# Performance work log

Hardware: AMD Instinct MI355X
Metric: run time of the kernel (lower is better)

Reference implementation:

```python
import jax, jax.numpy as jnp
import numpy as np
from jax import lax

D_MODEL = 200
N_LAYER = 12
NHEADS = 8
HEADDIM = 50
D_STATE = 64
D_INNER = 2 * D_MODEL            # 400
CONV_DIM = D_INNER + 2 * D_STATE  # 528 (ngroups=1)
D_IN_PROJ = 2 * D_INNER + 2 * D_STATE + NHEADS  # 936
D_CONV = 4
EPS = 1e-5


def rmsnorm(x, w):
    v = jnp.mean(jnp.square(x), axis=-1, keepdims=True)
    return x * lax.rsqrt(v + EPS) * w


def groupnorm(x, groups, g, b):
    B, C, H, W = x.shape
    xg = x.reshape(B, groups, C // groups, H, W)
    mu = jnp.mean(xg, axis=(2, 3, 4), keepdims=True)
    var = jnp.mean(jnp.square(xg - mu), axis=(2, 3, 4), keepdims=True)
    xn = ((xg - mu) * lax.rsqrt(var + EPS)).reshape(B, C, H, W)
    return xn * g[:, None, None] + b[:, None, None]


def patch_embed(x, pe_conv_w, proj_in_w, gn_g, gn_b, spec_w):
    b, c, l, d = x.shape
    # time path: 'b c l d' -> (b, 1, c*l, d), conv -> (b, 25, c*l, 8)
    time_x = x.reshape(b, 1, c * l, d)
    t = lax.conv_general_dilated(time_x, proj_in_w, (1, 25), ((0, 0), (24, 24)),
                                 dimension_numbers=('NCHW', 'OIHW', 'NCHW'))
    t = jax.nn.gelu(groupnorm(t, 5, gn_g, gn_b), approximate=False)
    time_emb = t.transpose(0, 2, 1, 3).reshape(b, c, l, D_MODEL)
    # freq path: rfft over patch dim, norm='forward'
    spec = jnp.abs(jnp.fft.rfft(x, axis=-1, norm='forward'))  # (b,c,l,101)
    spec_emb = jnp.einsum('bclf,df->bcld', spec, spec_w)
    patch = time_emb + spec_emb
    # depthwise 7x7 positional conv over (d, c, l)
    pos = lax.conv_general_dilated(patch.transpose(0, 3, 1, 2), pe_conv_w, (1, 1),
                                   ((3, 3), (3, 3)),
                                   dimension_numbers=('NCHW', 'OIHW', 'NCHW'),
                                   feature_group_count=D_MODEL)
    return patch + pos.transpose(0, 2, 3, 1)


def ssd_scan(xh, dt, B, C, A, D):
    # xh: (b,l,h,p)  dt: (b,l,h)  B,C: (b,l,n)  A,D: (h,)
    b, l, h, p = xh.shape

    def step(state, inp):
        x_t, dt_t, B_t, C_t = inp
        dA = jnp.exp(dt_t * A)  # (b,h)
        state = state * dA[:, :, None, None] + \
            (dt_t[:, :, None, None] * x_t[:, :, :, None]) * B_t[:, None, None, :]
        y = jnp.einsum('bhpn,bn->bhp', state, C_t)
        return state, y

    state0 = jnp.zeros((b, h, p, D_STATE), xh.dtype)
    _, ys = lax.scan(step, state0,
                     (xh.transpose(1, 0, 2, 3), dt.transpose(1, 0, 2),
                      B.transpose(1, 0, 2), C.transpose(1, 0, 2)))
    return ys.transpose(1, 0, 2, 3) + xh * D[None, None, :, None]


def mamba2(u, in_w, conv_w, conv_b, dt_bias, A_log, D, gn_w, out_w):
    b, l, _ = u.shape
    zxbcdt = u @ in_w.T  # (b,l,936)
    z = zxbcdt[..., :D_INNER]
    xBC = zxbcdt[..., D_INNER:D_INNER + CONV_DIM]
    dt = jax.nn.softplus(zxbcdt[..., D_INNER + CONV_DIM:] + dt_bias)  # (b,l,8)
    # causal depthwise conv1d, kernel 4
    xc = lax.conv_general_dilated(xBC.transpose(0, 2, 1), conv_w, (1,), ((D_CONV - 1, 0),),
                                  dimension_numbers=('NCH', 'OIH', 'NCH'),
                                  feature_group_count=CONV_DIM)
    xBC = jax.nn.silu((xc + conv_b[:, None]).transpose(0, 2, 1))
    x = xBC[..., :D_INNER].reshape(b, l, NHEADS, HEADDIM)
    Bm = xBC[..., D_INNER:D_INNER + D_STATE]
    Cm = xBC[..., D_INNER + D_STATE:]
    y = ssd_scan(x, dt, Bm, Cm, -jnp.exp(A_log), D).reshape(b, l, D_INNER)
    y = rmsnorm(y * jax.nn.silu(z), gn_w)  # RMSNormGated, norm_before_gate=False
    return y @ out_w.T


@jax.checkpoint
def layer(hidden, residual, norm_w, in_w, conv_w, conv_b, dt_bias, A_log, D, gn_w, out_w):
    residual = hidden + residual
    hidden = mamba2(rmsnorm(residual, norm_w), in_w, conv_w, conv_b, dt_bias, A_log, D, gn_w, out_w)
    return hidden, residual


def forward(x, pe_conv_w, proj_in_w, gn_g, gn_b, spec_w, norm_w, in_proj_w, conv_w, conv_b,
            dt_bias, A_log, D, gnorm_w, out_proj_w, norm_f_w, head_w, head_b):
    b, c, l, d = x.shape
    hidden = patch_embed(x, pe_conv_w, proj_in_w, gn_g, gn_b, spec_w).reshape(b, c * l, d)
    residual = jnp.zeros_like(hidden)
    for i in range(N_LAYER):
        hidden, residual = layer(hidden, residual, norm_w[i], in_proj_w[i], conv_w[i],
                                 conv_b[i], dt_bias[i], A_log[i], D[i], gnorm_w[i], out_proj_w[i])
    hidden = rmsnorm(hidden + residual, norm_f_w).reshape(b, c, l, d)
    return hidden @ head_w.T + head_b


def setup_inputs():
    key = jax.random.key(0)
    ks = jax.random.split(key, 12)
    B, CH, L, P = 16, 19, 30, 200

    def g(k, shape, scale):
        return jax.random.normal(k, shape, jnp.float32) * scale

    dt = jax.random.uniform(ks[8], (N_LAYER, NHEADS), jnp.float32, 1e-3, 0.1)
    return {
        'x': g(ks[0], (B, CH, L, P), 1.0),
        'pe_conv_w': g(ks[1], (D_MODEL, 1, 7, 7), 0.15),
        'proj_in_w': g(ks[2], (25, 1, 1, 49), 0.14),
        'gn_g': jnp.ones(25, jnp.float32),
        'gn_b': jnp.zeros(25, jnp.float32),
        'spec_w': g(ks[3], (D_MODEL, 101), 0.1),
        'norm_w': jnp.ones((N_LAYER, D_MODEL), jnp.float32),
        'in_proj_w': g(ks[4], (N_LAYER, D_IN_PROJ, D_MODEL), 0.07),
        'conv_w': g(ks[5], (N_LAYER, CONV_DIM, 1, D_CONV), 0.4),
        'conv_b': jnp.zeros((N_LAYER, CONV_DIM), jnp.float32),
        'dt_bias': jnp.log(jnp.expm1(dt)),
        'A_log': jnp.log(jax.random.uniform(ks[9], (N_LAYER, NHEADS), jnp.float32, 1.0, 16.0)),
        'D': jnp.ones((N_LAYER, NHEADS), jnp.float32),
        'gnorm_w': jnp.ones((N_LAYER, D_INNER), jnp.float32),
        'out_proj_w': g(ks[6], (N_LAYER, D_MODEL, D_INNER), 0.05),
        'norm_f_w': jnp.ones(D_MODEL, jnp.float32),
        'head_w': g(ks[7], (D_MODEL, D_MODEL), 0.07),
        'head_b': jnp.zeros(D_MODEL, jnp.float32),
    }


def reference(x, pe_conv_w, proj_in_w, gn_g, gn_b, spec_w, norm_w, in_proj_w, conv_w, conv_b,
              dt_bias, A_log, D, gnorm_w, out_proj_w, norm_f_w, head_w, head_b):
    return forward(x, pe_conv_w, proj_in_w, gn_g, gn_b, spec_w, norm_w, in_proj_w, conv_w,
                   conv_b, dt_bias, A_log, D, gnorm_w, out_proj_w, norm_f_w, head_w, head_b)
```

## Files before the change

### kernel.cpp

```cpp
#include <hip/hip_runtime.h>
#include <hip/hip_bf16.h>
#include <math.h>

#define D_MODEL   200
#define N_LAYER   12
#define NHEADS    8
#define HEADDIM   50
#define D_STATE   64
#define D_INNER   400
#define CONV_DIM  528
#define D_IN_PROJ 936
#define D_CONV    4
#define EPS       1e-5f

#define BATCH 16
#define CH    19
#define LLEN  30
#define SEQ   570
#define NTOK  9120
#define NFREQ 101

typedef __attribute__((ext_vector_type(8))) short s8v;
typedef __attribute__((ext_vector_type(4))) float f32x4;

// ... 166 lines not shown
}

__global__ __launch_bounds__(256) void time_conv_kernel(
    const float* __restrict__ x, const float* __restrict__ pw,
    float* __restrict__ traw)
{
    int br = blockIdx.x;
    __shared__ float xr[200];
    if (threadIdx.x < 200) xr[threadIdx.x] = x[(size_t)br * 200 + threadIdx.x];
    __syncthreads();
    if (threadIdx.x < 200) {
        int oc = threadIdx.x >> 3, j = threadIdx.x & 7;
        int start = j * 25 - 24;
        float acc = 0.f;
#pragma unroll
        for (int k = 0; k < 49; k++) {
            int d = start + k;
            if (d >= 0 && d < 200) acc = fmaf(xr[d], pw[oc * 49 + k], acc);
        }
        int b = br / SEQ, row = br % SEQ;
        traw[(((size_t)b * 25 + oc) * SEQ + row) * 8 + j] = acc;
    }
}

__global__ __launch_bounds__(256) void gn_stats_kernel(
    const float* __restrict__ traw, float* __restrict__ stats)
{
    int bg = blockIdx.x;
    int b = bg / 5, g = bg % 5;
    const float* base = traw + ((size_t)b * 25 + g * 5) * SEQ * 8;
    float s = 0.f, q = 0.f;
    for (int i = threadIdx.x; i < 5 * SEQ * 8; i += 256) {
        float v = base[i];
        s += v; q = fmaf(v, v, q);
    }
    __shared__ float rs[4], rq[4];
    int lane = threadIdx.x & 63, w = threadIdx.x >> 6;
#pragma unroll
    for (int o = 32; o; o >>= 1) { s += __shfl_xor(s, o, 64); q += __shfl_xor(q, o, 64); }
    if (lane == 0) { rs[w] = s; rq[w] = q; }
    __syncthreads();
    if (threadIdx.x == 0) {
        float S = rs[0] + rs[1] + rs[2] + rs[3];
        float Q = rq[0] + rq[1] + rq[2] + rq[3];
        float inv = 1.f / (5.f * SEQ * 8.f);
        float mean = S * inv;
        float var = Q * inv - mean * mean;
        stats[bg * 2] = mean;
        stats[bg * 2 + 1] = rsqrtf(var + EPS);
    }
}

__global__ __launch_bounds__(256) void gn_gelu_kernel(
    const float* __restrict__ traw, const float* __restrict__ stats,
    const float* __restrict__ gn_g, const float* __restrict__ gn_b,
    float* __restrict__ patch)
{
    int idx = blockIdx.x * 256 + threadIdx.x;
    if (idx >= NTOK * 200) return;
    int d = idx % 200;
    int row = (idx / 200) % SEQ;
    int b = idx / (200 * SEQ);
    int oc = d >> 3, j = d & 7;
    float v = traw[(((size_t)b * 25 + oc) * SEQ + row) * 8 + j];
    int g = oc / 5;
    float mean = stats[(b * 5 + g) * 2];
    float rstd = stats[(b * 5 + g) * 2 + 1];
    v = (v - mean) * rstd * gn_g[oc] + gn_b[oc];
    float ge = 0.5f * v * (1.f + erff(v * 0.70710678118654752f));
    patch[idx] = ge;
}

__global__ __launch_bounds__(256) void dft_init_kernel(float* __restrict__ CS)
{
    int idx = blockIdx.x * 256 + threadIdx.x;
    if (idx >= 202 * 200) return;
    int f = idx / 200, d = idx % 200;
    int fr = (f < NFREQ) ? f : (f - NFREQ);
    int m = (fr * d) % 200;
    float ang = -6.283185307179586f * (float)m * (1.f / 200.f);
    CS[idx] = (f < NFREQ) ? cosf(ang) : sinf(ang);
}

__global__ __launch_bounds__(256) void dft_init_bf_kernel(short* __restrict__ CS)
{
    int idx = blockIdx.x * 256 + threadIdx.x;
    if (idx >= 202 * 224) return;
    int f = idx / 224, d = idx - f * 224;
    short out = 0;
    if (d < 200) {
        int fr = (f < NFREQ) ? f : (f - NFREQ);
        int m = (fr * d) % 200;
        float ang = -6.283185307179586f * (float)m * (1.f / 200.f);
        out = f2bf((f < NFREQ) ? cosf(ang) : sinf(ang));
    }
    CS[idx] = out;
}

__global__ __launch_bounds__(256) void mag_kernel(
    const float* __restrict__ cs_out, float* __restrict__ magv)
{
    int idx = blockIdx.x * 256 + threadIdx.x;
    if (idx >= NTOK * NFREQ) return;
    int m = idx / NFREQ, f = idx % NFREQ;
    float re = cs_out[(size_t)m * 202 + f];
    float im = cs_out[(size_t)m * 202 + NFREQ + f];
    magv[idx] = sqrtf(re * re + im * im) * 0.005f;
}

__global__ __launch_bounds__(256) void mag_bf_kernel(
    const float* __restrict__ cs_out, short* __restrict__ magv)
{
    int idx = blockIdx.x * 256 + threadIdx.x;
    if (idx >= NTOK * 128) return;
    int m = idx >> 7, f = idx & 127;
    short out = 0;
    if (f < NFREQ) {
        float re = cs_out[(size_t)m * 202 + f];
        float im = cs_out[(size_t)m * 202 + NFREQ + f];
        out = f2bf(sqrtf(re * re + im * im) * 0.005f);
    }
    magv[idx] = out;
}

__global__ __launch_bounds__(256) void pe_conv3_kernel(
    const float* __restrict__ patch, const float* __restrict__ pw,
    float* __restrict__ hidden)
{
    int b = blockIdx.x, dc = blockIdx.y, ct = blockIdx.z;
    int d0 = dc * 16, c0 = ct * 4;
    __shared__ float pl[10 * 30 * 16];
    __shared__ float wl[49 * 16];
    int tid = threadIdx.x;
    int dd = tid & 15;
    int d = d0 + dd;

    for (int i = tid; i < 10 * 30 * 16; i += 256) {
        int ddl = i & 15, r = i >> 4;
        int l = r % 30, cr = r / 30;
        int cc = c0 + cr - 3, dl = d0 + ddl;
        pl[i] = (cc >= 0 && cc < CH && dl < 200)
                    ? patch[((size_t)(b * CH + cc) * LLEN + l) * 200 + dl] : 0.f;
    }
    for (int i = tid; i < 49 * 16; i += 256) {
        int k = i >> 4, dl = d0 + (i & 15);
        wl[i] = (dl < 200) ? pw[(size_t)dl * 49 + k] : 0.f;
    }
    __syncthreads();

    float wreg[49];
#pragma unroll
    for (int k = 0; k < 49; k++) wreg[k] = wl[k * 16 + dd];

    for (int o = tid; o < 4 * 30 * 16; o += 256) {
        int r2 = o >> 4;
        int l = r2 % 30, ci = r2 / 30;
        int c = c0 + ci;
        if (c >= CH) continue;
        float acc = pl[((ci + 3) * 30 + l) * 16 + dd];
#pragma unroll
        for (int i = 0; i < 7; i++) {
#pragma unroll
            for (int j = 0; j < 7; j++) {
                int ll = l + j - 3;
                if (ll < 0 || ll >= LLEN) continue;
                acc = fmaf(pl[((ci + i) * 30 + ll) * 16 + dd], wreg[i * 7 + j], acc);
            }
        }
        if (d < 200) hidden[((size_t)(b * CH + c) * LLEN + l) * 200 + d] = acc;
    }
}

__global__ __launch_bounds__(64) void add_rmsnorm_kernel(
    const float* __restrict__ hidden, float* __restrict__ residual,
    const float* __restrict__ wn, float* __restrict__ u,
    short* __restrict__ ubf, int first)
{
    int m = blockIdx.x;
    int lane = threadIdx.x;
    const float* hr = hidden + (size_t)m * 200;
    float* rr = residual + (size_t)m * 200;
    float v[4];
    float ss = 0.f;
#pragma unroll
    for (int i = 0; i < 4; i++) {
        int k = lane + i * 64;
        float xv = 0.f;
        if (k < 200) {
            xv = hr[k] + (first ? 0.f : rr[k]);
            rr[k] = xv;
        }
        v[i] = xv;
        ss = fmaf(xv, xv, ss);
    }
#pragma unroll
    for (int o = 32; o; o >>= 1) ss += __shfl_xor(ss, o, 64);
    float rstd = rsqrtf(ss * (1.f / 200.f) + EPS);
#pragma unroll
    for (int i = 0; i < 4; i++) {
        int k = lane + i * 64;
        float val = v[i] * rstd * ((k < 200) ? wn[k] : 0.f);
        if (k < 200 && u) u[(size_t)m * 200 + k] = val;
        if (ubf) {
            if (k < 200) ubf[(size_t)m * 224 + k] = f2bf(val);
            else if (k < 224) ubf[(size_t)m * 224 + k] = 0;
        }
    }
}

__global__ __launch_bounds__(256) void norm_dt_kernel(
    const float* __restrict__ hidden, float* __restrict__ residual,
    const float* __restrict__ wn, short* __restrict__ ubf,
    const float* __restrict__ Win, const float* __restrict__ dt_bias,
    float* __restrict__ dtb, int layer, int first)
{
    int m = blockIdx.x;
    int tid = threadIdx.x;
    __shared__ float su[200];
    __shared__ float rs[4];
    float xv = 0.f;
    if (tid < 200) {
        xv = hidden[(size_t)m * 200 + tid] + (first ? 0.f : residual[(size_t)m * 200 + tid]);
        residual[(size_t)m * 200 + tid] = xv;
    }
    float ss = xv * xv;
#pragma unroll
    for (int o = 32; o; o >>= 1) ss += __shfl_xor(ss, o, 64);
    int lane = tid & 63, w = tid >> 6;
    if (lane == 0) rs[w] = ss;
    __syncthreads();
    float rstd = rsqrtf((rs[0] + rs[1] + rs[2] + rs[3]) * (1.f / 200.f) + EPS);
    if (tid < 200) {
        float val = xv * rstd * wn[tid];
        su[tid] = val;
        ubf[(size_t)m * 224 + tid] = f2bf(val);
    } else if (tid < 224) {
        ubf[(size_t)m * 224 + tid] = 0;
    }
    __syncthreads();
    int h = tid >> 5, l = tid & 31;
    const float* wr = Win + (size_t)layer * D_IN_PROJ * 200 + (size_t)(928 + h) * 200;
    float s = 0.f;
    for (int k = l; k < 200; k += 32) s = fmaf(su[k], wr[k], s);
    s += __shfl_xor(s, 16, 32);
    s += __shfl_xor(s, 8, 32);
    s += __shfl_xor(s, 4, 32);
    s += __shfl_xor(s, 2, 32);
    s += __shfl_xor(s, 1, 32);
    if (l == 0) {
        float raw = s + dt_bias[layer * NHEADS + h];
        dtb[(size_t)m * NHEADS + h] = (raw > 20.f) ? raw : log1pf(expf(raw));
    }
}

__global__ __launch_bounds__(256) void dt_gemv_kernel(
    const float* __restrict__ u, const float* __restrict__ Win,
    const float* __restrict__ dt_bias, float* __restrict__ dtb, int layer)
{
    int tid = threadIdx.x;
    int tok = blockIdx.x * 4 + (tid >> 6);
    int head = (tid >> 3) & 7;
    int l8 = tid & 7;
    const float* ur = u + (size_t)tok * 200;
    const float* wr = Win + (size_t)layer * D_IN_PROJ * 200 + (size_t)(928 + head) * 200;
    float s = 0.f;
    for (int k = l8; k < 200; k += 8) s = fmaf(ur[k], wr[k], s);
    s += __shfl_xor(s, 1, 64);
    s += __shfl_xor(s, 2, 64);
    s += __shfl_xor(s, 4, 64);
    if (l8 == 0) {
        float raw = s + dt_bias[layer * NHEADS + head];
        dtb[(size_t)tok * NHEADS + head] = (raw > 20.f) ? raw : log1pf(expf(raw));
    }
}

__global__ __launch_bounds__(256) void dtconv2_kernel(
    const float* __restrict__ zxbcdt, const float* __restrict__ cw,
    const float* __restrict__ cb, float* __restrict__ xBC, int layer)
{
    int b = blockIdx.x, tt = blockIdx.y;
    int t0 = tt * 8;
    __shared__ float zs[11][528];
    const float* cwl = cw + (size_t)layer * CONV_DIM * 4;
    const float* cbl = cb + (size_t)layer * CONV_DIM;
    for (int i = threadIdx.x; i < 11 * 528; i += 256) {
        int r = i / 528, ch = i - r * 528;
        int t = t0 - 3 + r;
        zs[r][ch] = (t >= 0 && t < SEQ)
                        ? zxbcdt[(size_t)(b * SEQ + t) * D_IN_PROJ + D_INNER + ch] : 0.f;
    }
    __syncthreads();
    for (int o = threadIdx.x; o < 8 * 528; o += 256) {
        int tr = o / 528, ch = o - tr * 528;
        int t = t0 + tr;
        if (t >= SEQ) continue;
        float acc = cbl[ch];
#pragma unroll
        for (int k = 0; k < 4; k++)
            acc = fmaf(zs[tr + k][ch], cwl[ch * 4 + k], acc);
        xBC[(size_t)(b * SEQ + t) * CONV_DIM + ch] = acc / (1.f + expf(-acc));
    }
}

__global__ __launch_bounds__(512) void ssd_scanA_kernel(
    const float* __restrict__ xBC, const float* __restrict__ dtb,
    const float* __restrict__ A_log, const float* __restrict__ Dv,
    float* __restrict__ ylocal, float* __restrict__ Pref,
    float* __restrict__ Sbuf, float* __restrict__ Pd,
    int layer, int lchunk, int nchunk)
{
    int b = blockIdx.x, c = blockIdx.y;
    int tid = threadIdx.x;
    int h = tid >> 6, p = tid & 63;
    float A = -expf(A_log[layer * NHEADS + h]);
    float Dh = Dv[layer * NHEADS + h];

    __shared__ __align__(16) float sh[3][2][536];
    int t0 = c * lchunk;
    int npairs = lchunk >> 1;

    for (int j = 0; j < 2 && j < npairs; j++) {
        if (tid < 264) {
            int wch = (tid >= 132) ? 1 : 0;
            int fidx = tid - wch * 132;
            int tq = t0 + 2 * j + wch;
            float4 v = ((const float4*)(xBC + (size_t)(b * SEQ + tq) * CONV_DIM))[fidx];
            *(float4*)&sh[j][wch][fidx * 4] = v;
        } else if (tid < 280) {
            int e = tid - 264, tok = e >> 3, hd = e & 7;
            sh[j][tok][528 + hd] = dtb[(size_t)(b * SEQ + t0 + 2 * j + tok) * NHEADS + hd];
        }
    }
    __syncthreads();

    float s[64];
#pragma unroll
    for (int n = 0; n < 64; n++) s[n] = 0.f;
    float pacc = 1.f;

    for (int i = 0; i < npairs; i++) {
        int t = t0 + 2 * i;
        int buf = i % 3;
        int nb = (i + 2) % 3;
        bool pf = (i + 2 < npairs);
        float4 rx;
        float rdt = 0.f;
        int wch = 0, fidx = 0;
        if (pf) {
            if (tid < 264) {
                wch = (tid >= 132) ? 1 : 0;
                fidx = tid - wch * 132;
                int tq = t + 4 + wch;
                rx = ((const float4*)(xBC + (size_t)(b * SEQ + tq) * CONV_DIM))[fidx];
            } else if (tid < 280) {
                int e = tid - 264, tok = e >> 3, hd = e & 7;
                rdt = dtb[(size_t)(b * SEQ + t + 4 + tok) * NHEADS + hd];
            }
        }
#pragma unroll
        for (int k = 0; k < 2; k++) {
            float dtv = sh[buf][k][528 + h];
            float xp  = (p < HEADDIM) ? sh[buf][k][h * HEADDIM + p] : 0.f;
            float dA = __expf(dtv * A);
            float u  = dtv * xp;
            pacc *= dA;
            const float4* B4 = (const float4*)&sh[buf][k][D_INNER];
            const float4* C4 = (const float4*)&sh[buf][k][D_INNER + D_STATE];
            float y0 = 0.f, y1 = 0.f, y2 = 0.f, y3 = 0.f;
#pragma unroll
            for (int n4 = 0; n4 < 16; n4++) {
                float4 bq = B4[n4];
                float4 cq = C4[n4];
                float t0v = fmaf(s[4 * n4 + 0], dA, u * bq.x);
                float t1v = fmaf(s[4 * n4 + 1], dA, u * bq.y);
                float t2v = fmaf(s[4 * n4 + 2], dA, u * bq.z);
                float t3v = fmaf(s[4 * n4 + 3], dA, u * bq.w);
                s[4 * n4 + 0] = t0v; s[4 * n4 + 1] = t1v;
                s[4 * n4 + 2] = t2v; s[4 * n4 + 3] = t3v;
                y0 = fmaf(t0v, cq.x, y0);
                y1 = fmaf(t1v, cq.y, y1);
                y2 = fmaf(t2v, cq.z, y2);
                y3 = fmaf(t3v, cq.w, y3);
            }
            if (p < HEADDIM)
                ylocal[(size_t)(b * SEQ + t + k) * D_INNER + h * HEADDIM + p] =
                    fmaf(xp, Dh, (y0 + y1) + (y2 + y3));
            if (p == 0)
                Pref[(size_t)(b * SEQ + t + k) * NHEADS + h] = pacc;
        }
        if (pf) {
            if (tid < 264) *(float4*)&sh[nb][wch][fidx * 4] = rx;
            else if (tid < 280) { int e = tid - 264; sh[nb][e >> 3][528 + (e & 7)] = rdt; }
        }
        __syncthreads();
    }

    if (p < HEADDIM) {
        float* Sb = Sbuf + ((size_t)((b * NHEADS + h) * nchunk + c)) * (HEADDIM * 64)
                    + p * 64;
#pragma unroll
        for (int n4 = 0; n4 < 16; n4++)
            ((float4*)Sb)[n4] = make_float4(s[4 * n4], s[4 * n4 + 1],
                                            s[4 * n4 + 2], s[4 * n4 + 3]);
    }
    if (p == 0) Pd[(b * NHEADS + h) * nchunk + c] = pacc;
}

__global__ __launch_bounds__(512) void ssd_state_kernel(
    const float* __restrict__ xBC, const float* __restrict__ dtb,
    const float* __restrict__ A_log, float* __restrict__ Sbuf,
    float* __restrict__ Pd, int layer, int lchunk, int nchunk)
{
    int b = blockIdx.x, c = blockIdx.y;
    int tid = threadIdx.x;
    int h = tid >> 6, p = tid & 63;
    float A = -expf(A_log[layer * NHEADS + h]);

    __shared__ float sh[2][544];
    int t0 = c * lchunk, tend = t0 + lchunk;

    {
        const float* base = xBC + (size_t)(b * SEQ + t0) * CONV_DIM;
        sh[0][tid] = base[tid];
        if (tid < 24) {
            int e2 = 512 + tid;
            sh[0][e2] = (e2 < 528) ? base[e2]
                                   : dtb[(size_t)(b * SEQ + t0) * NHEADS + (e2 - 528)];
        }
    }
    __syncthreads();

    float s[64];
#pragma unroll
    for (int n = 0; n < 64; n++) s[n] = 0.f;
    float pacc = 1.f;

    for (int t = t0; t < tend; t++) {
        int cur = (t - t0) & 1, nxt = cur ^ 1;
        float pf0 = 0.f, pf1 = 0.f;
        if (t + 1 < tend) {
            const float* base = xBC + (size_t)(b * SEQ + t + 1) * CONV_DIM;
            pf0 = base[tid];
            if (tid < 24) {
                int e2 = 512 + tid;
                pf1 = (e2 < 528) ? base[e2]
                                 : dtb[(size_t)(b * SEQ + t + 1) * NHEADS + (e2 - 528)];
            }
        }
        float dtv = sh[cur][528 + h];
        float xp  = (p < HEADDIM) ? sh[cur][h * HEADDIM + p] : 0.f;
        float dA = __expf(dtv * A);
        float u  = dtv * xp;
        pacc *= dA;
        const float4* B4 = (const float4*)&sh[cur][D_INNER];
#pragma unroll
        for (int n4 = 0; n4 < 16; n4++) {
            float4 bq = B4[n4];
            s[4 * n4 + 0] = fmaf(s[4 * n4 + 0], dA, u * bq.x);
            s[4 * n4 + 1] = fmaf(s[4 * n4 + 1], dA, u * bq.y);
            s[4 * n4 + 2] = fmaf(s[4 * n4 + 2], dA, u * bq.z);
            s[4 * n4 + 3] = fmaf(s[4 * n4 + 3], dA, u * bq.w);
        }
        if (t + 1 < tend) {
            sh[nxt][tid] = pf0;
            if (tid < 24) sh[nxt][512 + tid] = pf1;
        }
        __syncthreads();
    }

    if (p < HEADDIM) {
        float* Sb = Sbuf + ((size_t)((b * NHEADS + h) * nchunk + c)) * (HEADDIM * 64)
                    + p * 64;
#pragma unroll
        for (int n4 = 0; n4 < 16; n4++)
            ((float4*)Sb)[n4] = make_float4(s[4 * n4], s[4 * n4 + 1],
                                            s[4 * n4 + 2], s[4 * n4 + 3]);
    }
    if (p == 0) Pd[(b * NHEADS + h) * nchunk + c] = pacc;
}

__global__ __launch_bounds__(256) void ssd_scan2b_kernel(
    float* __restrict__ Sbuf, const float* __restrict__ Pd, int nchunk)
{
    int bh = blockIdx.x;
    int e = blockIdx.y * 256 + threadIdx.x;
    if (e >= HEADDIM * 64) return;
    float* base = Sbuf + (size_t)bh * nchunk * (HEADDIM * 64) + e;
    const float* pd = Pd + bh * nchunk;
    float cur = 0.f;
    for (int c = 0; c < nchunk; c++) {
        float l = base[(size_t)c * (HEADDIM * 64)];
        base[(size_t)c * (HEADDIM * 64)] = cur;
        cur = fmaf(pd[c], cur, l);
    }
}

__global__ __launch_bounds__(512) void ssd_corr_kernel(
    const float* __restrict__ xBC, const float* __restrict__ zxbcdt,
    const float* __restrict__ ylocal, const float* __restrict__ Pref,
    const float* __restrict__ Sbuf, const float* __restrict__ gw,
    short* __restrict__ ybf, int layer, int lchunk, int nchunk)
{
    int b = blockIdx.x, c = blockIdx.y;
    int tid = threadIdx.x;
    int h = tid >> 6, p = tid & 63;
    float gval = (p < HEADDIM) ? gw[(size_t)layer * D_INNER + h * HEADDIM + p] : 0.f;

    __shared__ __align__(16) float Cst[2][2][64];
    __shared__ float pfs[2][2][8];
    __shared__ float red[2][2][8];
    int t0 = c * lchunk;
    int npairs = lchunk >> 1;

    float s0[64];
    if (p < HEADDIM) {
        const float* Sb = Sbuf + ((size_t)((b * NHEADS + h) * nchunk + c)) * (HEADDIM * 64)
                          + p * 64;
#pragma unroll
        for (int n4 = 0; n4 < 16; n4++) {
            float4 v = ((const float4*)Sb)[n4];
            s0[4 * n4] = v.x; s0[4 * n4 + 1] = v.y;
            s0[4 * n4 + 2] = v.z; s0[4 * n4 + 3] = v.w;
        }
    } else {
#pragma unroll
        for (int n = 0; n < 64; n++) s0[n] = 0.f;
    }

    int col = h * HEADDIM + ((p < HEADDIM) ? p : 0);

    if (tid < 128) {
        int k = tid >> 6, n = tid & 63;
        Cst[0][k][n] = xBC[(size_t)(b * SEQ + t0 + k) * CONV_DIM + D_INNER + D_STATE + n];
    } else if (tid < 144) {
        int e = tid - 128, k = e >> 3, hd = e & 7;
        pfs[0][k][hd] = Pref[(size_t)(b * SEQ + t0 + k) * NHEADS + hd];
    }
    float ylr[2], zvr[2];
#pragma unroll
    for (int k = 0; k < 2; k++) {
        ylr[k] = ylocal[(size_t)(b * SEQ + t0 + k) * D_INNER + col];
        zvr[k] = zxbcdt[(size_t)(b * SEQ + t0 + k) * D_IN_PROJ + col];
    }
    __syncthreads();

    for (int i = 0; i < npairs; i++) {
        int t = t0 + 2 * i;
        int buf = i & 1, nb = buf ^ 1;
        bool pf = (i + 1 < npairs);
        float rc = 0.f, rpf = 0.f, yln[2], zvn[2];
        if (pf) {
            if (tid < 128) {
                int k = tid >> 6, n = tid & 63;
                rc = xBC[(size_t)(b * SEQ + t + 2 + k) * CONV_DIM + D_INNER + D_STATE + n];
            } else if (tid < 144) {
                int e = tid - 128, k = e >> 3, hd = e & 7;
                rpf = Pref[(size_t)(b * SEQ + t + 2 + k) * NHEADS + hd];
            }
#pragma unroll
            for (int k = 0; k < 2; k++) {
                yln[k] = ylocal[(size_t)(b * SEQ + t + 2 + k) * D_INNER + col];
                zvn[k] = zxbcdt[(size_t)(b * SEQ + t + 2 + k) * D_IN_PROJ + col];
            }
        }
        float g0 = 0.f, g1 = 0.f;
#pragma unroll
        for (int k = 0; k < 2; k++) {
            const float4* C4 = (const float4*)&Cst[buf][k][0];
            float c0 = 0.f, c1 = 0.f, c2 = 0.f, c3 = 0.f;
#pragma unroll
            for (int n4 = 0; n4 < 16; n4++) {
                float4 cq = C4[n4];
                c0 = fmaf(s0[4 * n4 + 0], cq.x, c0);
                c1 = fmaf(s0[4 * n4 + 1], cq.y, c1);
                c2 = fmaf(s0[4 * n4 + 2], cq.z, c2);
                c3 = fmaf(s0[4 * n4 + 3], cq.w, c3);
            }
            float corr = (c0 + c1) + (c2 + c3);
            float yv = fmaf(pfs[buf][k][h], corr, ylr[k]);
            float zv = zvr[k];
            float gg = yv * (zv / (1.f + expf(-zv)));
            gg = (p < HEADDIM) ? gg : 0.f;
            if (k == 0) g0 = gg; else g1 = gg;
        }
        float gs0 = g0 * g0, gs1 = g1 * g1;
#pragma unroll
        for (int o = 32; o; o >>= 1) {
            gs0 += __shfl_xor(gs0, o, 64);
            gs1 += __shfl_xor(gs1, o, 64);
        }
        if (p == 0) { red[buf][0][h] = gs0; red[buf][1][h] = gs1; }
        if (pf) {
            if (tid < 128) { int k = tid >> 6, n = tid & 63; Cst[nb][k][n] = rc; }
            else if (tid < 144) { int e = tid - 128; pfs[nb][e >> 3][e & 7] = rpf; }
            ylr[0] = yln[0]; ylr[1] = yln[1];
            zvr[0] = zvn[0]; zvr[1] = zvn[1];
        }
        __syncthreads();
        float tot0 = (red[buf][0][0] + red[buf][0][1]) + (red[buf][0][2] + red[buf][0][3]) +
                     (red[buf][0][4] + red[buf][0][5]) + (red[buf][0][6] + red[buf][0][7]);
        float tot1 = (red[buf][1][0] + red[buf][1][1]) + (red[buf][1][2] + red[buf][1][3]) +
                     (red[buf][1][4] + red[buf][1][5]) + (red[buf][1][6] + red[buf][1][7]);
        float rstd0 = rsqrtf(tot0 * (1.f / D_INNER) + EPS);
        float rstd1 = rsqrtf(tot1 * (1.f / D_INNER) + EPS);
        size_t row0 = (size_t)(b * SEQ + t) * 416;
        size_t row1 = (size_t)(b * SEQ + t + 1) * 416;
        if (p < HEADDIM) {
            ybf[row0 + h * HEADDIM + p] = f2bf(g0 * rstd0 * gval);
            ybf[row1 + h * HEADDIM + p] = f2bf(g1 * rstd1 * gval);
        } else {
            int widx = h * 14 + (p - HEADDIM);
            if (widx < 16) {
                ybf[row0 + 400 + widx] = 0;
                ybf[row1 + 400 + widx] = 0;
            }
        }
    }
}

__global__ __launch_bounds__(512) void ssd_out_kernel(
    const float* __restrict__ xBC, const float* __restrict__ dtb,
    const float* __restrict__ A_log, const float* __restrict__ Dv,
    const float* __restrict__ Sbuf, float* __restrict__ y,
    int layer, int lchunk, int nchunk)
{
    int b = blockIdx.x, c = blockIdx.y;
    int tid = threadIdx.x;
    int h = tid >> 6, p = tid & 63;
    float A = -expf(A_log[layer * NHEADS + h]);
    float Dh = Dv[layer * NHEADS + h];

    __shared__ float sh[2][544];
    int t0 = c * lchunk, tend = t0 + lchunk;

    {
        const float* base = xBC + (size_t)(b * SEQ + t0) * CONV_DIM;
        sh[0][tid] = base[tid];
        if (tid < 24) {
            int e2 = 512 + tid;
            sh[0][e2] = (e2 < 528) ? base[e2]
                                   : dtb[(size_t)(b * SEQ + t0) * NHEADS + (e2 - 528)];
        }
    }

    float s[64];
    if (p < HEADDIM) {
        const float* Sb = Sbuf + ((size_t)((b * NHEADS + h) * nchunk + c)) * (HEADDIM * 64)
                          + p * 64;
#pragma unroll
        for (int n4 = 0; n4 < 16; n4++) {
            float4 v = ((const float4*)Sb)[n4];
            s[4 * n4] = v.x; s[4 * n4 + 1] = v.y; s[4 * n4 + 2] = v.z; s[4 * n4 + 3] = v.w;
        }
    } else {
#pragma unroll
        for (int n = 0; n < 64; n++) s[n] = 0.f;
    }
    __syncthreads();

    for (int t = t0; t < tend; t++) {
        int cur = (t - t0) & 1, nxt = cur ^ 1;
        float pf0 = 0.f, pf1 = 0.f;
        if (t + 1 < tend) {
            const float* base = xBC + (size_t)(b * SEQ + t + 1) * CONV_DIM;
            pf0 = base[tid];
            if (tid < 24) {
                int e2 = 512 + tid;
                pf1 = (e2 < 528) ? base[e2]
                                 : dtb[(size_t)(b * SEQ + t + 1) * NHEADS + (e2 - 528)];
            }
        }
        float dtv = sh[cur][528 + h];
        float xp  = (p < HEADDIM) ? sh[cur][h * HEADDIM + p] : 0.f;
        float dA = __expf(dtv * A);
        float u  = dtv * xp;
        const float4* B4 = (const float4*)&sh[cur][D_INNER];
        const float4* C4 = (const float4*)&sh[cur][D_INNER + D_STATE];
        float y0 = 0.f, y1 = 0.f, y2 = 0.f, y3 = 0.f;
#pragma unroll
        for (int n4 = 0; n4 < 16; n4++) {
            float4 bq = B4[n4];
            float4 cq = C4[n4];
            float t0v = fmaf(s[4 * n4 + 0], dA, u * bq.x);
            float t1v = fmaf(s[4 * n4 + 1], dA, u * bq.y);
            float t2v = fmaf(s[4 * n4 + 2], dA, u * bq.z);
            float t3v = fmaf(s[4 * n4 + 3], dA, u * bq.w);
            s[4 * n4 + 0] = t0v; s[4 * n4 + 1] = t1v;
            s[4 * n4 + 2] = t2v; s[4 * n4 + 3] = t3v;
            y0 = fmaf(t0v, cq.x, y0);
            y1 = fmaf(t1v, cq.y, y1);
            y2 = fmaf(t2v, cq.z, y2);
            y3 = fmaf(t3v, cq.w, y3);
        }
        if (p < HEADDIM) {
            float yv = (y0 + y1) + (y2 + y3);
            y[(size_t)(b * SEQ + t) * D_INNER + h * HEADDIM + p] = fmaf(xp, Dh, yv);
        }
        if (t + 1 < tend) {
            sh[nxt][tid] = pf0;
            if (tid < 24) sh[nxt][512 + tid] = pf1;
        }
        __syncthreads();
    }
}

__global__ __launch_bounds__(256) void gate_norm_kernel(
    float* __restrict__ y, const float* __restrict__ zxbcdt,
    const float* __restrict__ gw, short* __restrict__ ybf, int layer)
{
    int m = blockIdx.x;
    __shared__ float buf[D_INNER];
    __shared__ float red[4];
    const float* z = zxbcdt + (size_t)m * D_IN_PROJ;
    float* yr = y + (size_t)m * D_INNER;
    const float* gwl = gw + (size_t)layer * D_INNER;
    float ss = 0.f;
    for (int k = threadIdx.x; k < D_INNER; k += 256) {
        float zv = z[k];
        float sz = zv / (1.f + expf(-zv));
        float g = yr[k] * sz;
        buf[k] = g;
        ss = fmaf(g, g, ss);
    }
    int lane = threadIdx.x & 63, w = threadIdx.x >> 6;
#pragma unroll
    for (int o = 32; o; o >>= 1) ss += __shfl_xor(ss, o, 64);
    if (lane == 0) red[w] = ss;
    __syncthreads();
    float tot = red[0] + red[1] + red[2] + red[3];
    float rstd = rsqrtf(tot * (1.f / D_INNER) + EPS);
    for (int k = threadIdx.x; k < 416; k += 256) {
        if (k < D_INNER) {
            float v = buf[k] * rstd * gwl[k];
            yr[k] = v;
            if (ybf) ybf[(size_t)m * 416 + k] = f2bf(v);
        } else if (ybf) {
            ybf[(size_t)m * 416 + k] = 0;
        }
    }
}

extern "C" void kernel_launch(void* const* d_in, const int* in_sizes, int n_in,
                              void* d_out, int out_size, void* d_ws, size_t ws_size,
                              hipStream_t stream)
{
    const float* x         = (const float*)d_in[0];
    const float* pe_conv_w = (const float*)d_in[1];
    const float* proj_in_w = (const float*)d_in[2];
    const float* gn_g      = (const float*)d_in[3];
    const float* gn_b      = (const float*)d_in[4];
    const float* spec_w    = (const float*)d_in[5];
    const float* norm_w    = (const float*)d_in[6];
    const float* in_proj_w = (const float*)d_in[7];
    const float* conv_w    = (const float*)d_in[8];
    const float* conv_b    = (const float*)d_in[9];
    const float* dt_bias   = (const float*)d_in[10];
    const float* A_log     = (const float*)d_in[11];
    const float* Dv        = (const float*)d_in[12];
    const float* gnorm_w   = (const float*)d_in[13];
    const float* out_proj_w= (const float*)d_in[14];
    const float* norm_f_w  = (const float*)d_in[15];
    const float* head_w    = (const float*)d_in[16];
    const float* head_b    = (const float*)d_in[17];
    float* out = (float*)d_out;
    float* ws  = (float*)d_ws;

    const size_t needA = 31650304ull * sizeof(float);
    int fast = (ws_size >= needA) ? 1 : 0;

    int nchunk, lchunk;
    float *residual = ws, *hidden = ws + 1824000;
    float *zxbcdt, *xBC, *dtb, *Sbuf, *Pd;
    float *ubuf = nullptr, *ybuf = nullptr, *ybuf_s = nullptr, *Pref = nullptr;
    short *w_in_bf = nullptr, *w_out_bf = nullptr, *w_head_bf = nullptr,
          *w_spec_bf = nullptr, *csmat_bf = nullptr, *x_bf = nullptr,
          *ubuf_bf = nullptr, *ybuf_bf = nullptr, *magb_bf = nullptr;

    if (fast) {
        nchunk = 15; lchunk = 38;
        zxbcdt = ws + 3648000;
        xBC    = ws + 12184320;
        dtb    = ws + 16999680;
        Sbuf   = ws + 17072640;
        Pd     = ws + 23216640;
        short* pool = (short*)(ws + 23218560);
        w_in_bf   = pool;
        w_out_bf  = pool + 2515968;
        w_head_bf = pool + 3514368;
        w_spec_bf = pool + 3559168;
        ubuf_bf   = pool + 3584768;
        ybuf_bf   = pool + 5627648;
        ybuf_s    = ws + 27929344;
        Pref      = ws + 31577344;
        csmat_bf  = (short*)(Sbuf + 4000000);
        x_bf      = (short*)(Sbuf + 4100000);
        magb_bf   = (short*)(Sbuf + 5200000);
    } else {
        nchunk = 6; lchunk = 95;
        ubuf   = ws + 3648000;
        zxbcdt = ws + 5472000;
        xBC    = ws + 14008320;
        dtb    = ws + 18823680;
        ybuf   = ws + 18896640;
        Sbuf   = ws + 1824000;
        Pd     = ws + 5470000;
    }

    float* traw  = fast ? Sbuf : ybuf;
    float* patch = zxbcdt;
    float* csout = fast ? (Sbuf + 2000000) : (xBC + 50000);
    float* csmat = xBC;
    float* magb  = fast ? nullptr : (xBC + 2000000);
    float* stats = dtb;

    if (fast) {
        cast_pad_kernel<<<(12 * 936 * 224 + 255) / 256, 256, 0, stream>>>(
            in_proj_w, w_in_bf, 12 * 936, 200, 224);
        cast_pad_kernel<<<(12 * 200 * 416 + 255) / 256, 256, 0, stream>>>(
            out_proj_w, w_out_bf, 12 * 200, 400, 416);
        cast_pad_kernel<<<(200 * 224 + 255) / 256, 256, 0, stream>>>(
            head_w, w_head_bf, 200, 200, 224);
        cast_pad_kernel<<<(200 * 128 + 255) / 256, 256, 0, stream>>>(
            spec_w, w_spec_bf, 200, 101, 128);
        cast_pad_kernel<<<(9120 * 224 + 255) / 256, 256, 0, stream>>>(
            x, x_bf, 9120, 200, 224);
        dft_init_bf_kernel<<<(202 * 224 + 255) / 256, 256, 0, stream>>>(csmat_bf);
    } else {
        dft_init_kernel<<<(202 * 200 + 255) / 256, 256, 0, stream>>>(csmat);
    }

    time_conv_kernel<<<NTOK, 256, 0, stream>>>(x, proj_in_w, traw);
    gn_stats_kernel<<<80, 256, 0, stream>>>(traw, stats);
    gn_gelu_kernel<<<(NTOK * 200 + 255) / 256, 256, 0, stream>>>(traw, stats, gn_g, gn_b, patch);
    if (fast) {
        gemm_bf16<<<dim3(2, 72), 256, 0, stream>>>(x_bf, csmat_bf, nullptr, csout,
                                                   NTOK, 202, 224, 0);
        mag_bf_kernel<<<(NTOK * 128 + 255) / 256, 256, 0, stream>>>(csout, magb_bf);
        gemm_bf16<<<dim3(2, 72), 256, 0, stream>>>(magb_bf, w_spec_bf, nullptr, patch,
                                                   NTOK, 200, 128, 1);
    } else {
        gemm_nt<<<dim3(2, 72), 256, 0, stream>>>(x, csmat, nullptr, csout, NTOK, 202, 200, 0);
        mag_kernel<<<(NTOK * NFREQ + 255) / 256, 256, 0, stream>>>(csout, magb);
        gemm_nt<<<dim3(2, 72), 256, 0, stream>>>(magb, spec_w, nullptr, patch,
                                                 NTOK, 200, NFREQ, 1);
    }
    pe_conv3_kernel<<<dim3(16, 13, 5), 256, 0, stream>>>(patch, pe_conv_w, hidden);

    for (int i = 0; i < N_LAYER; i++) {
        if (fast) {
            norm_dt_kernel<<<NTOK, 256, 0, stream>>>(hidden, residual, norm_w + i * 200,
                                                     ubuf_bf, in_proj_w, dt_bias, dtb,
                                                     i, (i == 0) ? 1 : 0);
            gemm_bf16<<<dim3(8, 72), 256, 0, stream>>>(
                ubuf_bf, w_in_bf + (size_t)i * 936 * 224, nullptr, zxbcdt,
                NTOK, D_IN_PROJ, 224, 0);
        } else {
            add_rmsnorm_kernel<<<NTOK, 64, 0, stream>>>(hidden, residual, norm_w + i * 200,
                                                        ubuf, nullptr, (i == 0) ? 1 : 0);
            dt_gemv_kernel<<<NTOK / 4, 256, 0, stream>>>(ubuf, in_proj_w, dt_bias, dtb, i);
            gemm_nt<<<dim3(8, 72), 256, 0, stream>>>(
                ubuf, in_proj_w + (size_t)i * D_IN_PROJ * 200, nullptr, zxbcdt,
                NTOK, D_IN_PROJ, 200, 0);
        }
        dtconv2_kernel<<<dim3(16, 72), 256, 0, stream>>>(zxbcdt, conv_w, conv_b, xBC, i);
        {
            dim3 g(BATCH, nchunk);
            if (fast) {
                ssd_scanA_kernel<<<g, 512, 0, stream>>>(xBC, dtb, A_log, Dv,
                                                        ybuf_s, Pref, Sbuf, Pd,
                                                        i, lchunk, nchunk);
                ssd_scan2b_kernel<<<dim3(BATCH * NHEADS, 13), 256, 0, stream>>>(Sbuf, Pd, nchunk);
                ssd_corr_kernel<<<g, 512, 0, stream>>>(
                    xBC, zxbcdt, ybuf_s, Pref, Sbuf, gnorm_w, ybuf_bf, i, lchunk, nchunk);
                gemm_bf16<<<dim3(2, 72), 256, 0, stream>>>(
                    ybuf_bf, w_out_bf + (size_t)i * 200 * 416, nullptr, hidden,
                    NTOK, 200, 416, 0);
            } else {
                ssd_state_kernel<<<g, 512, 0, stream>>>(xBC, dtb, A_log, Sbuf, Pd,
                                                        i, lchunk, nchunk);
                ssd_scan2b_kernel<<<dim3(BATCH * NHEADS, 13), 256, 0, stream>>>(Sbuf, Pd, nchunk);
                ssd_out_kernel<<<g, 512, 0, stream>>>(xBC, dtb, A_log, Dv, Sbuf, ybuf,
                                                      i, lchunk, nchunk);
                gate_norm_kernel<<<NTOK, 256, 0, stream>>>(ybuf, zxbcdt, gnorm_w, nullptr, i);
                gemm_nt<<<dim3(2, 72), 256, 0, stream>>>(
                    ybuf, out_proj_w + (size_t)i * 200 * D_INNER, nullptr, hidden,
                    NTOK, 200, D_INNER, 0);
            }
        }
    }

    add_rmsnorm_kernel<<<NTOK, 64, 0, stream>>>(hidden, residual, norm_f_w,
                                                fast ? nullptr : ubuf,
                                                fast ? ubuf_bf : nullptr, 0);
    if (fast) {
        gemm_bf16<<<dim3(2, 72), 256, 0, stream>>>(ubuf_bf, w_head_bf, head_b, out,
                                                   NTOK, 200, 224, 0);
    } else {
        gemm_nt<<<dim3(2, 72), 256, 0, stream>>>(ubuf, head_w, head_b, out,
                                                 NTOK, 200, 200, 0);
    }
}
```

Before: 2.565 ms.

## Split SSD scan and correction kernels into per-head single-wave blocks

Result: slower. 2.829 ms (+10.3%).

```diff
diff --git a/kernel.cpp b/kernel.cpp
--- a/kernel.cpp
+++ b/kernel.cpp
@@ -492,97 +492,73 @@
     }
 }
 
-__global__ __launch_bounds__(512) void ssd_scanA_kernel(
+__global__ __launch_bounds__(64) void ssd_scanA2_kernel(
     const float* __restrict__ xBC, const float* __restrict__ dtb,
     const float* __restrict__ A_log, const float* __restrict__ Dv,
     float* __restrict__ ylocal, float* __restrict__ Pref,
     float* __restrict__ Sbuf, float* __restrict__ Pd,
     int layer, int lchunk, int nchunk)
 {
-    int b = blockIdx.x, c = blockIdx.y;
-    int tid = threadIdx.x;
-    int h = tid >> 6, p = tid & 63;
+    int b = blockIdx.x, h = blockIdx.y, c = blockIdx.z;
+    int p = threadIdx.x;
     float A = -expf(A_log[layer * NHEADS + h]);
     float Dh = Dv[layer * NHEADS + h];
-
-    __shared__ __align__(16) float sh[3][2][536];
+    __shared__ __align__(16) float bc[2][128];
+
     int t0 = c * lchunk;
-    int npairs = lchunk >> 1;
-
-    for (int j = 0; j < 2 && j < npairs; j++) {
-        if (tid < 264) {
-            int wch = (tid >= 132) ? 1 : 0;
-            int fidx = tid - wch * 132;
-            int tq = t0 + 2 * j + wch;
-            float4 v = ((const float4*)(xBC + (size_t)(b * SEQ + tq) * CONV_DIM))[fidx];
-            *(float4*)&sh[j][wch][fidx * 4] = v;
-        } else if (tid < 280) {
-            int e = tid - 264, tok = e >> 3, hd = e & 7;
-            sh[j][tok][528 + hd] = dtb[(size_t)(b * SEQ + t0 + 2 * j + tok) * NHEADS + hd];
-        }
-    }
-    __syncthreads();
+    float xv[2], bv[2], cv[2], dtv[2];
+#pragma unroll
+    for (int j = 0; j < 2; j++) {
+        const float* row = xBC + (size_t)(b * SEQ + t0 + j) * CONV_DIM;
+        xv[j] = (p < HEADDIM) ? row[h * HEADDIM + p] : 0.f;
+        bv[j] = row[D_INNER + p];
+        cv[j] = row[D_INNER + D_STATE + p];
+        dtv[j] = dtb[(size_t)(b * SEQ + t0 + j) * NHEADS + h];
+    }
 
     float s[64];
 #pragma unroll
     for (int n = 0; n < 64; n++) s[n] = 0.f;
     float pacc = 1.f;
 
-    for (int i = 0; i < npairs; i++) {
-        int t = t0 + 2 * i;
-        int buf = i % 3;
-        int nb = (i + 2) % 3;
-        bool pf = (i + 2 < npairs);
-        float4 rx;
-        float rdt = 0.f;
-        int wch = 0, fidx = 0;
-        if (pf) {
-            if (tid < 264) {
-                wch = (tid >= 132) ? 1 : 0;
-                fidx = tid - wch * 132;
-                int tq = t + 4 + wch;
-                rx = ((const float4*)(xBC + (size_t)(b * SEQ + tq) * CONV_DIM))[fidx];
-            } else if (tid < 280) {
-                int e = tid - 264, tok = e >> 3, hd = e & 7;
-                rdt = dtb[(size_t)(b * SEQ + t + 4 + tok) * NHEADS + hd];
-            }
-        }
-#pragma unroll
-        for (int k = 0; k < 2; k++) {
-            float dtv = sh[buf][k][528 + h];
-            float xp  = (p < HEADDIM) ? sh[buf][k][h * HEADDIM + p] : 0.f;
-            float dA = __expf(dtv * A);
-            float u  = dtv * xp;
-            pacc *= dA;
-            const float4* B4 = (const float4*)&sh[buf][k][D_INNER];
-            const float4* C4 = (const float4*)&sh[buf][k][D_INNER + D_STATE];
-            float y0 = 0.f, y1 = 0.f, y2 = 0.f, y3 = 0.f;
-#pragma unroll
-            for (int n4 = 0; n4 < 16; n4++) {
-                float4 bq = B4[n4];
-                float4 cq = C4[n4];
-                float t0v = fmaf(s[4 * n4 + 0], dA, u * bq.x);
-                float t1v = fmaf(s[4 * n4 + 1], dA, u * bq.y);
-                float t2v = fmaf(s[4 * n4 + 2], dA, u * bq.z);
-                float t3v = fmaf(s[4 * n4 + 3], dA, u * bq.w);
-                s[4 * n4 + 0] = t0v; s[4 * n4 + 1] = t1v;
-                s[4 * n4 + 2] = t2v; s[4 * n4 + 3] = t3v;
-                y0 = fmaf(t0v, cq.x, y0);
-                y1 = fmaf(t1v, cq.y, y1);
-                y2 = fmaf(t2v, cq.z, y2);
-                y3 = fmaf(t3v, cq.w, y3);
-            }
-            if (p < HEADDIM)
-                ylocal[(size_t)(b * SEQ + t + k) * D_INNER + h * HEADDIM + p] =
-                    fmaf(xp, Dh, (y0 + y1) + (y2 + y3));
-            if (p == 0)
-                Pref[(size_t)(b * SEQ + t + k) * NHEADS + h] = pacc;
-        }
-        if (pf) {
-            if (tid < 264) *(float4*)&sh[nb][wch][fidx * 4] = rx;
-            else if (tid < 280) { int e = tid - 264; sh[nb][e >> 3][528 + (e & 7)] = rdt; }
-        }
-        __syncthreads();
+    for (int i = 0; i < lchunk; i++) {
+        int sl = i & 1;
+        float xc = xv[sl], dtc = dtv[sl];
+        bc[sl][p] = bv[sl];
+        bc[sl][64 + p] = cv[sl];
+        if (i + 2 < lchunk) {
+            const float* row = xBC + (size_t)(b * SEQ + t0 + i + 2) * CONV_DIM;
+            xv[sl] = (p < HEADDIM) ? row[h * HEADDIM + p] : 0.f;
+            bv[sl] = row[D_INNER + p];
+            cv[sl] = row[D_INNER + D_STATE + p];
+            dtv[sl] = dtb[(size_t)(b * SEQ + t0 + i + 2) * NHEADS + h];
+        }
+        float dA = __expf(dtc * A);
+        float u = dtc * xc;
+        pacc *= dA;
+        const float4* B4 = (const float4*)&bc[sl][0];
+        const float4* C4 = (const float4*)&bc[sl][64];
+        float y0 = 0.f, y1 = 0.f, y2 = 0.f, y3 = 0.f;
+#pragma unroll
+        for (int n4 = 0; n4 < 16; n4++) {
+            float4 bq = B4[n4];
+            float4 cq = C4[n4];
+            float t0v = fmaf(s[4 * n4 + 0], dA, u * bq.x);
+            float t1v = fmaf(s[4 * n4 + 1], dA, u * bq.y);
+            float t2v = fmaf(s[4 * n4 + 2], dA, u * bq.z);
+            float t3v = fmaf(s[4 * n4 + 3], dA, u * bq.w);
+            s[4 * n4 + 0] = t0v; s[4 * n4 + 1] = t1v;
+            s[4 * n4 + 2] = t2v; s[4 * n4 + 3] = t3v;
+            y0 = fmaf(t0v, cq.x, y0);
+            y1 = fmaf(t1v, cq.y, y1);
+            y2 = fmaf(t2v, cq.z, y2);
+            y3 = fmaf(t3v, cq.w, y3);
+        }
+        if (p < HEADDIM)
+            ylocal[(size_t)(b * SEQ + t0 + i) * D_INNER + h * HEADDIM + p] =
+                fmaf(xc, Dh, (y0 + y1) + (y2 + y3));
+        if (p == 0)
+            Pref[(size_t)(b * SEQ + t0 + i) * NHEADS + h] = pacc;
     }
 
     if (p < HEADDIM) {
@@ -685,22 +661,16 @@
     }
 }
 
-__global__ __launch_bounds__(512) void ssd_corr_kernel(
+__global__ __launch_bounds__(64) void ssd_corrB_kernel(
     const float* __restrict__ xBC, const float* __restrict__ zxbcdt,
-    const float* __restrict__ ylocal, const float* __restrict__ Pref,
-    const float* __restrict__ Sbuf, const float* __restrict__ gw,
-    short* __restrict__ ybf, int layer, int lchunk, int nchunk)
-{
-    int b = blockIdx.x, c = blockIdx.y;
-    int tid = threadIdx.x;
-    int h = tid >> 6, p = tid & 63;
-    float gval = (p < HEADDIM) ? gw[(size_t)layer * D_INNER + h * HEADDIM + p] : 0.f;
-
-    __shared__ __align__(16) float Cst[2][2][64];
-    __shared__ float pfs[2][2][8];
-    __shared__ float red[2][2][8];
+    float* __restrict__ g, const float* __restrict__ Pref,
+    float* __restrict__ Psum, const float* __restrict__ Sbuf,
+    int lchunk, int nchunk)
+{
+    int b = blockIdx.x, h = blockIdx.y, c = blockIdx.z;
+    int p = threadIdx.x;
+    __shared__ __align__(16) float cs[2][64];
     int t0 = c * lchunk;
-    int npairs = lchunk >> 1;
 
     float s0[64];
     if (p < HEADDIM) {
@@ -718,93 +688,66 @@
     }
 
     int col = h * HEADDIM + ((p < HEADDIM) ? p : 0);
-
-    if (tid < 128) {
-        int k = tid >> 6, n = tid & 63;
-        Cst[0][k][n] = xBC[(size_t)(b * SEQ + t0 + k) * CONV_DIM + D_INNER + D_STATE + n];
-    } else if (tid < 144) {
-        int e = tid - 128, k = e >> 3, hd = e & 7;
-        pfs[0][k][hd] = Pref[(size_t)(b * SEQ + t0 + k) * NHEADS + hd];
-    }
-    float ylr[2], zvr[2];
-#pragma unroll
-    for (int k = 0; k < 2; k++) {
-        ylr[k] = ylocal[(size_t)(b * SEQ + t0 + k) * D_INNER + col];
-        zvr[k] = zxbcdt[(size_t)(b * SEQ + t0 + k) * D_IN_PROJ + col];
-    }
-    __syncthreads();
-
-    for (int i = 0; i < npairs; i++) {
-        int t = t0 + 2 * i;
-        int buf = i & 1, nb = buf ^ 1;
-        bool pf = (i + 1 < npairs);
-        float rc = 0.f, rpf = 0.f, yln[2], zvn[2];
-        if (pf) {
-            if (tid < 128) {
-                int k = tid >> 6, n = tid & 63;
-                rc = xBC[(size_t)(b * SEQ + t + 2 + k) * CONV_DIM + D_INNER + D_STATE + n];
-            } else if (tid < 144) {
-                int e = tid - 128, k = e >> 3, hd = e & 7;
-                rpf = Pref[(size_t)(b * SEQ + t + 2 + k) * NHEADS + hd];
-            }
-#pragma unroll
-            for (int k = 0; k < 2; k++) {
-                yln[k] = ylocal[(size_t)(b * SEQ + t + 2 + k) * D_INNER + col];
-                zvn[k] = zxbcdt[(size_t)(b * SEQ + t + 2 + k) * D_IN_PROJ + col];
-            }
-        }
-        float g0 = 0.f, g1 = 0.f;
-#pragma unroll
-        for (int k = 0; k < 2; k++) {
-            const float4* C4 = (const float4*)&Cst[buf][k][0];
-            float c0 = 0.f, c1 = 0.f, c2 = 0.f, c3 = 0.f;
-#pragma unroll
-            for (int n4 = 0; n4 < 16; n4++) {
-                float4 cq = C4[n4];
-                c0 = fmaf(s0[4 * n4 + 0], cq.x, c0);
-                c1 = fmaf(s0[4 * n4 + 1], cq.y, c1);
-                c2 = fmaf(s0[4 * n4 + 2], cq.z, c2);
-                c3 = fmaf(s0[4 * n4 + 3], cq.w, c3);
-            }
-            float corr = (c0 + c1) + (c2 + c3);
-            float yv = fmaf(pfs[buf][k][h], corr, ylr[k]);
-            float zv = zvr[k];
-            float gg = yv * (zv / (1.f + expf(-zv)));
-            gg = (p < HEADDIM) ? gg : 0.f;
-            if (k == 0) g0 = gg; else g1 = gg;
-        }
-        float gs0 = g0 * g0, gs1 = g1 * g1;
-#pragma unroll
-        for (int o = 32; o; o >>= 1) {
-            gs0 += __shfl_xor(gs0, o, 64);
-            gs1 += __shfl_xor(gs1, o, 64);
-        }
-        if (p == 0) { red[buf][0][h] = gs0; red[buf][1][h] = gs1; }
-        if (pf) {
-            if (tid < 128) { int k = tid >> 6, n = tid & 63; Cst[nb][k][n] = rc; }
-            else if (tid < 144) { int e = tid - 128; pfs[nb][e >> 3][e & 7] = rpf; }
-            ylr[0] = yln[0]; ylr[1] = yln[1];
-            zvr[0] = zvn[0]; zvr[1] = zvn[1];
-        }
-        __syncthreads();
-        float tot0 = (red[buf][0][0] + red[buf][0][1]) + (red[buf][0][2] + red[buf][0][3]) +
-                     (red[buf][0][4] + red[buf][0][5]) + (red[buf][0][6] + red[buf][0][7]);
-        float tot1 = (red[buf][1][0] + red[buf][1][1]) + (red[buf][1][2] + red[buf][1][3]) +
-                     (red[buf][1][4] + red[buf][1][5]) + (red[buf][1][6] + red[buf][1][7]);
-        float rstd0 = rsqrtf(tot0 * (1.f / D_INNER) + EPS);
-        float rstd1 = rsqrtf(tot1 * (1.f / D_INNER) + EPS);
-        size_t row0 = (size_t)(b * SEQ + t) * 416;
-        size_t row1 = (size_t)(b * SEQ + t + 1) * 416;
-        if (p < HEADDIM) {
-            ybf[row0 + h * HEADDIM + p] = f2bf(g0 * rstd0 * gval);
-            ybf[row1 + h * HEADDIM + p] = f2bf(g1 * rstd1 * gval);
-        } else {
-            int widx = h * 14 + (p - HEADDIM);
-            if (widx < 16) {
-                ybf[row0 + 400 + widx] = 0;
-                ybf[row1 + 400 + widx] = 0;
-            }
-        }
+    float cv[2], yv[2], zv[2], pf[2];
+#pragma unroll
+    for (int j = 0; j < 2; j++) {
+        size_t tok = (size_t)(b * SEQ + t0 + j);
+        cv[j] = xBC[tok * CONV_DIM + D_INNER + D_STATE + p];
+        yv[j] = g[tok * D_INNER + col];
+        zv[j] = zxbcdt[tok * D_IN_PROJ + col];
+        pf[j] = Pref[tok * NHEADS + h];
+    }
+
+    for (int i = 0; i < lchunk; i++) {
+        int sl = i & 1;
+        size_t tok = (size_t)(b * SEQ + t0 + i);
+        float yc = yv[sl], zc = zv[sl], pc = pf[sl];
+        cs[sl][p] = cv[sl];
+        if (i + 2 < lchunk) {
+            size_t tok2 = (size_t)(b * SEQ + t0 + i + 2);
+            cv[sl] = xBC[tok2 * CONV_DIM + D_INNER + D_STATE + p];
+            yv[sl] = g[tok2 * D_INNER + col];
+            zv[sl] = zxbcdt[tok2 * D_IN_PROJ + col];
+            pf[sl] = Pref[tok2 * NHEADS + h];
+        }
+        const float4* C4 = (const float4*)&cs[sl][0];
+        float c0 = 0.f, c1 = 0.f, c2 = 0.f, c3 = 0.f;
+#pragma unroll
+        for (int n4 = 0; n4 < 16; n4++) {
+            float4 cq = C4[n4];
+            c0 = fmaf(s0[4 * n4 + 0], cq.x, c0);
+            c1 = fmaf(s0[4 * n4 + 1], cq.y, c1);
+            c2 = fmaf(s0[4 * n4 + 2], cq.z, c2);
+            c3 = fmaf(s0[4 * n4 + 3], cq.w, c3);
+        }
+        float yvv = fmaf(pc, (c0 + c1) + (c2 + c3), yc);
+        float gg = yvv * (zc / (1.f + expf(-zc)));
+        gg = (p < HEADDIM) ? gg : 0.f;
+        float gs = gg * gg;
+#pragma unroll
+        for (int o = 32; o; o >>= 1) gs += __shfl_xor(gs, o, 64);
+        if (p < HEADDIM) g[tok * D_INNER + col] = gg;
+        if (p == 0) Psum[tok * NHEADS + h] = gs;
+    }
+}
+
+__global__ __launch_bounds__(64) void gate_finish_kernel(
+    const float* __restrict__ g, const float* __restrict__ Psum,
+    const float* __restrict__ gw, short* __restrict__ ybf, int layer)
+{
+    int m = blockIdx.x;
+    int lane = threadIdx.x;
+    const float* ps = Psum + (size_t)m * NHEADS;
+    float tot = (ps[0] + ps[1]) + (ps[2] + ps[3]) + (ps[4] + ps[5]) + (ps[6] + ps[7]);
+    float rstd = rsqrtf(tot * (1.f / D_INNER) + EPS);
+    const float* gwl = gw + (size_t)layer * D_INNER;
+#pragma unroll
+    for (int j = 0; j < 7; j++) {
+        int k = lane + j * 64;
+        if (k < D_INNER)
+            ybf[(size_t)m * 416 + k] = f2bf(g[(size_t)m * D_INNER + k] * rstd * gwl[k]);
+        else if (k < 416)
+            ybf[(size_t)m * 416 + k] = 0;
     }
 }
 
@@ -955,13 +898,14 @@
     float* out = (float*)d_out;
     float* ws  = (float*)d_ws;
 
-    const size_t needA = 31650304ull * sizeof(float);
+    const size_t needA = 31723264ull * sizeof(float);
     int fast = (ws_size >= needA) ? 1 : 0;
 
     int nchunk, lchunk;
     float *residual = ws, *hidden = ws + 1824000;
     float *zxbcdt, *xBC, *dtb, *Sbuf, *Pd;
-    float *ubuf = nullptr, *ybuf = nullptr, *ybuf_s = nullptr, *Pref = nullptr;
+    float *ubuf = nullptr, *ybuf = nullptr, *ybuf_s = nullptr, *Pref = nullptr,
+          *Psum = nullptr;
     short *w_in_bf = nullptr, *w_out_bf = nullptr, *w_head_bf = nullptr,
           *w_spec_bf = nullptr, *csmat_bf = nullptr, *x_bf = nullptr,
           *ubuf_bf = nullptr, *ybuf_bf = nullptr, *magb_bf = nullptr;
@@ -982,6 +926,7 @@
         ybuf_bf   = pool + 5627648;
         ybuf_s    = ws + 27929344;
         Pref      = ws + 31577344;
+        Psum      = ws + 31650304;
         csmat_bf  = (short*)(Sbuf + 4000000);
         x_bf      = (short*)(Sbuf + 4100000);
         magb_bf   = (short*)(Sbuf + 5200000);
@@ -1053,29 +998,29 @@
                 NTOK, D_IN_PROJ, 200, 0);
         }
         dtconv2_kernel<<<dim3(16, 72), 256, 0, stream>>>(zxbcdt, conv_w, conv_b, xBC, i);
-        {
+        if (fast) {
+            dim3 g(BATCH, NHEADS, nchunk);
+            ssd_scanA2_kernel<<<g, 64, 0, stream>>>(xBC, dtb, A_log, Dv,
+                                                    ybuf_s, Pref, Sbuf, Pd,
+                                                    i, lchunk, nchunk);
+            ssd_scan2b_kernel<<<dim3(BATCH * NHEADS, 13), 256, 0, stream>>>(Sbuf, Pd, nchunk);
+            ssd_corrB_kernel<<<g, 64, 0, stream>>>(xBC, zxbcdt, ybuf_s, Pref, Psum,
+                                                   Sbuf, lchunk, nchunk);
+            gate_finish_kernel<<<NTOK, 64, 0, stream>>>(ybuf_s, Psum, gnorm_w, ybuf_bf, i);
+            gemm_bf16<<<dim3(2, 72), 256, 0, stream>>>(
+                ybuf_bf, w_out_bf + (size_t)i * 200 * 416, nullptr, hidden,
+                NTOK, 200, 416, 0);
+        } else {
             dim3 g(BATCH, nchunk);
-            if (fast) {
-                ssd_scanA_kernel<<<g, 512, 0, stream>>>(xBC, dtb, A_log, Dv,
-                                                        ybuf_s, Pref, Sbuf, Pd,
-                                                        i, lchunk, nchunk);
-                ssd_scan2b_kernel<<<dim3(BATCH * NHEADS, 13), 256, 0, stream>>>(Sbuf, Pd, nchunk);
-                ssd_corr_kernel<<<g, 512, 0, stream>>>(
-                    xBC, zxbcdt, ybuf_s, Pref, Sbuf, gnorm_w, ybuf_bf, i, lchunk, nchunk);
-                gemm_bf16<<<dim3(2, 72), 256, 0, stream>>>(
-                    ybuf_bf, w_out_bf + (size_t)i * 200 * 416, nullptr, hidden,
-                    NTOK, 200, 416, 0);
-            } else {
-                ssd_state_kernel<<<g, 512, 0, stream>>>(xBC, dtb, A_log, Sbuf, Pd,
-                                                        i, lchunk, nchunk);
-                ssd_scan2b_kernel<<<dim3(BATCH * NHEADS, 13), 256, 0, stream>>>(Sbuf, Pd, nchunk);
-                ssd_out_kernel<<<g, 512, 0, stream>>>(xBC, dtb, A_log, Dv, Sbuf, ybuf,
-                                                      i, lchunk, nchunk);
-                gate_norm_kernel<<<NTOK, 256, 0, stream>>>(ybuf, zxbcdt, gnorm_w, nullptr, i);
-                gemm_nt<<<dim3(2, 72), 256, 0, stream>>>(
-                    ybuf, out_proj_w + (size_t)i * 200 * D_INNER, nullptr, hidden,
-                    NTOK, 200, D_INNER, 0);
-            }
+            ssd_state_kernel<<<g, 512, 0, stream>>>(xBC, dtb, A_log, Sbuf, Pd,
+                                                    i, lchunk, nchunk);
+            ssd_scan2b_kernel<<<dim3(BATCH * NHEADS, 13), 256, 0, stream>>>(Sbuf, Pd, nchunk);
+            ssd_out_kernel<<<g, 512, 0, stream>>>(xBC, dtb, A_log, Dv, Sbuf, ybuf,
+                                                  i, lchunk, nchunk);
+            gate_norm_kernel<<<NTOK, 256, 0, stream>>>(ybuf, zxbcdt, gnorm_w, nullptr, i);
+            gemm_nt<<<dim3(2, 72), 256, 0, stream>>>(
+                ybuf, out_proj_w + (size_t)i * 200 * D_INNER, nullptr, hidden,
+                NTOK, 200, D_INNER, 0);
         }
     }
 
```
